# Kernel optimization log

Measured on AMD Instinct MI355X. Metric: run time of the kernel, lower is better.

Reference implementation:

```python
import jax, jax.numpy as jnp
import numpy as np

NUM_EDGE_TYPES = 38
NUM_NODE_TYPES = 4
HIDDEN = 64
HOPS = 4
N_NODES = 100_000
N_EDGES = 1_600_000


def setup_inputs() -> dict:
    key = jax.random.key(0)
    ks = jax.random.split(key, 7)
    in_dim = NUM_EDGE_TYPES + 2 * NUM_NODE_TYPES  # 46
    return {
        "edge_index": jax.random.randint(ks[0], (2, N_EDGES), 0, N_NODES),
        "edge_type": jax.random.randint(ks[1], (N_EDGES,), 0, NUM_EDGE_TYPES),
        "node_type": jax.random.randint(ks[2], (N_NODES,), 0, NUM_NODE_TYPES),
        "W1": jax.random.normal(ks[3], (in_dim, HIDDEN), dtype=jnp.float32) * 0.1,
        "b1": jax.random.normal(ks[4], (HIDDEN,), dtype=jnp.float32) * 0.1,
        "W2": jax.random.normal(ks[5], (HIDDEN, 1), dtype=jnp.float32) * 0.1,
        "b2": jax.random.normal(ks[6], (1,), dtype=jnp.float32) * 0.1,
    }


def reference(edge_index, edge_type, node_type, W1, b1, W2, b2):
    src, dst = edge_index[0], edge_index[1]  # PyG: x_j = x[edge_index[0]], aggregate at edge_index[1]
    head_type = node_type[src]
    tail_type = node_type[dst]
    # Linear over concat of three one-hots == sum of three gathered weight rows + bias.
    h = (W1[edge_type]
         + W1[NUM_EDGE_TYPES + head_type]
         + W1[NUM_EDGE_TYPES + NUM_NODE_TYPES + tail_type]
         + b1)                                   # [E, HIDDEN]
    h = jax.nn.gelu(h)
    edge_emb = jax.nn.sigmoid(h @ W2 + b2)       # [E, 1]

    num_nodes = node_type.shape[0]
    aggr = jnp.zeros((num_nodes, 1), dtype=edge_emb.dtype)
    for _ in range(HOPS):
        msg = aggr[src] + edge_emb               # gather + add, [E, 1]
        aggr = jax.ops.segment_sum(msg, dst, num_segments=num_nodes)  # scatter-add
    return aggr
```

## Files before the change

kernel.cpp:

```cpp
#include <hip/hip_runtime.h>

#define NUM_EDGE_TYPES 38
#define NUM_NODE_TYPES 4
#define HIDDEN 64
#define TABLE_SIZE (NUM_EDGE_TYPES * NUM_NODE_TYPES * NUM_NODE_TYPES)
#define SRC_BITS 17
#define SRC_MASK ((1 << SRC_BITS) - 1)
#define BSHIFT 8
#define BNODES 256
#define MAXB 512
#define CHUNK 4096
#define PB 512
#define HB 1024
#define CAPC 6144

__global__ void partition_kernel(const int* __restrict__ src, const int* __restrict__ dst,
                                 const int* __restrict__ etype, int* __restrict__ cursor,
                                 int* __restrict__ pack, int E, int nbk, int cap) {
    __shared__ int hist[MAXB];
    __shared__ int locCur[MAXB];
    for (int i = threadIdx.x; i < nbk; i += PB) hist[i] = 0;
    __syncthreads();
    int start = blockIdx.x * CHUNK;
    int end = min(start + CHUNK, E);
    if (end - start == CHUNK) {
        int j = start + threadIdx.x;
        int d[8], s[8], et[8], slot[8];
#pragma unroll
        for (int k = 0; k < 8; ++k) d[k] = dst[j + k * PB];
#pragma unroll
        for (int k = 0; k < 8; ++k) atomicAdd(&hist[d[k] >> BSHIFT], 1);
        __syncthreads();
        for (int i = threadIdx.x; i < nbk; i += PB) {
            int h = hist[i];
            locCur[i] = h ? i * cap + atomicAdd(&cursor[i], h) : 0;
        }
        __syncthreads();
#pragma unroll
        for (int k = 0; k < 8; ++k) s[k] = src[j + k * PB];
#pragma unroll
        for (int k = 0; k < 8; ++k) et[k] = etype[j + k * PB];
#pragma unroll
        for (int k = 0; k < 8; ++k) slot[k] = atomicAdd(&locCur[d[k] >> BSHIFT], 1);
#pragma unroll
        for (int k = 0; k < 8; ++k)
            pack[slot[k]] = (et[k] << (SRC_BITS + 8)) | ((d[k] & (BNODES - 1)) << SRC_BITS) | s[k];
    } else {
        for (int j = start + threadIdx.x; j < end; j += PB)
            atomicAdd(&hist[dst[j] >> BSHIFT], 1);
        __syncthreads();
        for (int i = threadIdx.x; i < nbk; i += PB) {
            int h = hist[i];
            locCur[i] = h ? i * cap + atomicAdd(&cursor[i], h) : 0;
        }
        __syncthreads();
        for (int j = start + threadIdx.x; j < end; j += PB) {
            int d = dst[j];
            int slot = atomicAdd(&locCur[d >> BSHIFT], 1);
            pack[slot] = (etype[j] << (SRC_BITS + 8)) | ((d & (BNODES - 1)) << SRC_BITS) | src[j];
        }
    }
}

__global__ void sort_base_kernel(int* __restrict__ pack, const int* __restrict__ cursor,
                                 const int* __restrict__ ntype,
                                 const float* __restrict__ W1, const float* __restrict__ b1,
                                 const float* __restrict__ W2, const float* __restrict__ b2,
                                 float* __restrict__ base, int* __restrict__ nodeOffG,
                                 int N, int cap) {
    __shared__ int sortedL[CAPC];
    __shared__ float tbl[TABLE_SIZE];
    __shared__ int nodeCnt[BNODES];
    __shared__ int nodeOff[BNODES + 1];
    __shared__ unsigned char ntLoc[BNODES];
    int b = blockIdx.x;
    int node0 = b << BSHIFT;
    int tid = threadIdx.x;
    int st = b * cap;
    int c = cursor[b];
    c = min(c, cap);

    if (tid < TABLE_SIZE) {
        int i = tid;
        int et = i >> 4, ht = (i >> 2) & 3, tt = i & 3;
        const float* r0 = W1 + et * HIDDEN;
        const float* r1 = W1 + (NUM_EDGE_TYPES + ht) * HIDDEN;
        const float* r2 = W1 + (NUM_EDGE_TYPES + NUM_NODE_TYPES + tt) * HIDDEN;
        float acc = b2[0];
#pragma unroll 8
        for (int k = 0; k < HIDDEN; ++k) {
            float h = r0[k] + r1[k] + r2[k] + b1[k];
            float u = 0.7978845608028654f * (h + 0.044715f * h * h * h);
            float g = 0.5f * h * (1.0f + tanhf(u));
            acc += g * W2[k];
        }
        tbl[i] = 1.0f / (1.0f + expf(-acc));
    }
    if (tid < BNODES) {
        nodeCnt[tid] = 0;
        int n = node0 + tid;
        ntLoc[tid] = (n < N) ? (unsigned char)ntype[n] : 0;
    }
    __syncthreads();

    for (int j = tid; j < c; j += HB)
        atomicAdd(&nodeCnt[(pack[st + j] >> SRC_BITS) & (BNODES - 1)], 1);
    __syncthreads();

    if (tid < 64) {
        int lane = tid;
        int v0 = nodeCnt[lane * 4], v1 = nodeCnt[lane * 4 + 1];
        int v2 = nodeCnt[lane * 4 + 2], v3 = nodeCnt[lane * 4 + 3];
        int s = v0 + v1 + v2 + v3;
        int inc = s;
        for (int d = 1; d < 64; d <<= 1) {
            int t = __shfl_up(inc, d, 64);
            if (lane >= d) inc += t;
        }
        int excl = inc - s;
        nodeOff[lane * 4]     = excl;
        nodeOff[lane * 4 + 1] = excl + v0;
        nodeOff[lane * 4 + 2] = excl + v0 + v1;
        nodeOff[lane * 4 + 3] = excl + v0 + v1 + v2;
        if (lane == 63) nodeOff[BNODES] = inc;
    }
    __syncthreads();
    if (tid < BNODES) nodeCnt[tid] = 0;
    __syncthreads();

    for (int j = tid; j < c; j += HB) {
        int p = pack[st + j];
        int dl = (p >> SRC_BITS) & (BNODES - 1);
        int r = atomicAdd(&nodeCnt[dl], 1);
        sortedL[nodeOff[dl] + r] = p;
    }
    __syncthreads();

    for (int j = tid; j < c; j += HB) pack[st + j] = sortedL[j];
    if (tid < BNODES) nodeOffG[(b << BSHIFT) + tid] = nodeOff[tid];

    int node = tid >> 2, l = tid & 3;
    int lo = nodeOff[node], hi = nodeOff[node + 1];
    int nt = ntLoc[node];
    float s = 0.0f;
    int j = lo + l;
    for (; j + 4 < hi; j += 8) {
        int p0 = sortedL[j], p1 = sortedL[j + 4];
        int i0 = ((((unsigned)p0) >> (SRC_BITS + 8)) << 4) | (ntype[p0 & SRC_MASK] << 2) | nt;
        int i1 = ((((unsigned)p1) >> (SRC_BITS + 8)) << 4) | (ntype[p1 & SRC_MASK] << 2) | nt;
        s += tbl[i0] + tbl[i1];
    }
    if (j < hi) {
        int p = sortedL[j];
        s += tbl[((((unsigned)p) >> (SRC_BITS + 8)) << 4) | (ntype[p & SRC_MASK] << 2) | nt];
    }
    s += __shfl_xor(s, 1, 64);
    s += __shfl_xor(s, 2, 64);
    int n = node0 + node;
    if (l == 0 && n < N) base[n] = s;
}

__global__ void hop_csr_kernel(const int* __restrict__ pack, const int* __restrict__ nodeOffG,
                               const int* __restrict__ cursor, const float* __restrict__ base,
                               const float* __restrict__ prev, float* __restrict__ out,
                               int N, int cap) {
    __shared__ int off[BNODES + 1];
    int b = blockIdx.x;
    int tid = threadIdx.x;
    int st = b * cap;
    if (tid < BNODES) off[tid] = nodeOffG[(b << BSHIFT) + tid];
    if (tid == 0) off[BNODES] = min(cursor[b], cap);
    __syncthreads();
    int node = tid >> 2, l = tid & 3;
    int lo = off[node], hi = off[node + 1];
    float s = 0.0f;
    int j = st + lo + l;
    int hiG = st + hi;
    for (; j + 4 < hiG; j += 8) {
        int p0 = pack[j], p1 = pack[j + 4];
        s += prev[p0 & SRC_MASK] + prev[p1 & SRC_MASK];
    }
    if (j < hiG) s += prev[pack[j] & SRC_MASK];
    s += __shfl_xor(s, 1, 64);
    s += __shfl_xor(s, 2, 64);
    int n = (b << BSHIFT) + node;
    if (l == 0 && n < N) out[n] = base[n] + s;
}

__global__ void table_kernel(const float* __restrict__ W1, const float* __restrict__ b1,
                             const float* __restrict__ W2, const float* __restrict__ b2,
                             float* __restrict__ table) {
    int i = blockIdx.x * blockDim.x + threadIdx.x;
    if (i >= TABLE_SIZE) return;
    int et = i >> 4, ht = (i >> 2) & 3, tt = i & 3;
    const float* r0 = W1 + et * HIDDEN;
    const float* r1 = W1 + (NUM_EDGE_TYPES + ht) * HIDDEN;
    const float* r2 = W1 + (NUM_EDGE_TYPES + NUM_NODE_TYPES + tt) * HIDDEN;
    float acc = b2[0];
#pragma unroll 8
    for (int k = 0; k < HIDDEN; ++k) {
        float h = r0[k] + r1[k] + r2[k] + b1[k];
        float u = 0.7978845608028654f * (h + 0.044715f * h * h * h);
        float g = 0.5f * h * (1.0f + tanhf(u));
        acc += g * W2[k];
    }
    table[i] = 1.0f / (1.0f + expf(-acc));
}

__global__ void edge_base_kernel(const int* __restrict__ src, const int* __restrict__ dst,
                                 const int* __restrict__ etype, const int* __restrict__ ntype,
                                 const float* __restrict__ table, float* __restrict__ base, int E) {
    __shared__ float tbl[TABLE_SIZE];
    for (int i = threadIdx.x; i < TABLE_SIZE; i += blockDim.x) tbl[i] = table[i];
    __syncthreads();
    int e = blockIdx.x * blockDim.x + threadIdx.x;
    if (e >= E) return;
    int s = src[e];
    int d = dst[e];
    int idx = (etype[e] << 4) | (ntype[s] << 2) | ntype[d];
    atomicAdd(base + d, tbl[idx]);
}

__global__ void copy_kernel(const float* __restrict__ in, float* __restrict__ out, int N) {
    int i = blockIdx.x * blockDim.x + threadIdx.x;
    if (i < N) out[i] = in[i];
}

__global__ void edge_hop_kernel(const int* __restrict__ src, const int* __restrict__ dst,
                                const float* __restrict__ prev, float* __restrict__ next, int E) {
    int e = blockIdx.x * blockDim.x + threadIdx.x;
    if (e >= E) return;
    atomicAdd(next + dst[e], prev[src[e]]);
}

extern "C" void kernel_launch(void* const* d_in, const int* in_sizes, int n_in,
                              void* d_out, int out_size, void* d_ws, size_t ws_size,
                              hipStream_t stream) {
    const int* edge_index = (const int*)d_in[0];
    const int* etype      = (const int*)d_in[1];
    const int* ntype      = (const int*)d_in[2];
    const float* W1       = (const float*)d_in[3];
    const float* b1       = (const float*)d_in[4];
    const float* W2       = (const float*)d_in[5];
    const float* b2       = (const float*)d_in[6];

    const int E = in_sizes[1];
    const int N = in_sizes[2];
    const int* src = edge_index;
    const int* dst = edge_index + E;
    float* out = (float*)d_out;

    const int nbk = (N + BNODES - 1) >> BSHIFT;
    const int nChunks = (E + CHUNK - 1) / CHUNK;

    int cap = ((E / (nbk > 0 ? nbk : 1)) * 3 / 2 + 255) & ~255;
    if (cap < 512) cap = 512;
    size_t packElems = (size_t)nbk * cap;

    size_t need = (packElems + MAXB + (size_t)nbk * BNODES + (size_t)3 * N) * 4 + 256;

    if (ws_size >= need && nbk <= MAXB && cap <= CAPC) {
        int* pack     = (int*)d_ws;
        int* cursor   = pack + packElems;
        int* nodeOffG = cursor + MAXB;
        float* base   = (float*)(nodeOffG + (size_t)nbk * BNODES);
        float* bufA   = base + N;
        float* bufB   = bufA + N;

        hipMemsetAsync(cursor, 0, (size_t)nbk * sizeof(int), stream);

        partition_kernel<<<nChunks, PB, 0, stream>>>(src, dst, etype, cursor, pack, E, nbk, cap);
        sort_base_kernel<<<nbk, HB, 0, stream>>>(pack, cursor, ntype, W1, b1, W2, b2,
                                                 base, nodeOffG, N, cap);
        hop_csr_kernel<<<nbk, HB, 0, stream>>>(pack, nodeOffG, cursor, base, base, bufA, N, cap);
        hop_csr_kernel<<<nbk, HB, 0, stream>>>(pack, nodeOffG, cursor, base, bufA, bufB, N, cap);
        hop_csr_kernel<<<nbk, HB, 0, stream>>>(pack, nodeOffG, cursor, base, bufB, out, N, cap);
    } else {
        float* table = (float*)d_ws;
        float* base  = table + 1024;
        float* bufA  = base + N;
        float* bufB  = bufA + N;
        const int eb = (E + 255) / 256;
        const int nb = (N + 255) / 256;

        hipMemsetAsync(base, 0, (size_t)N * sizeof(float), stream);
        table_kernel<<<(TABLE_SIZE + 255) / 256, 256, 0, stream>>>(W1, b1, W2, b2, table);

        edge_base_kernel<<<eb, 256, 0, stream>>>(src, dst, etype, ntype, table, base, E);
        copy_kernel<<<nb, 256, 0, stream>>>(base, bufA, N);
        edge_hop_kernel<<<eb, 256, 0, stream>>>(src, dst, base, bufA, E);
        copy_kernel<<<nb, 256, 0, stream>>>(base, bufB, N);
        edge_hop_kernel<<<eb, 256, 0, stream>>>(src, dst, bufA, bufB, E);
        copy_kernel<<<nb, 256, 0, stream>>>(base, out, N);
        edge_hop_kernel<<<eb, 256, 0, stream>>>(src, dst, bufB, out, E);
    }
}
```

Before: 155.1 us.

## Fuse sort, base and hop kernels into one cooperative persistent kernel

Replaces the sort_base kernel and three hop_csr launches with a single cooperative kernel that keeps each bucket's sorted edge list in shared memory and separates hops with grid-wide syncs. This removes three kernel launches and the global write and re-read of the sorted pack and node offsets. In exchange it relies on cooperative launch support and all 391 blocks being co-resident (512 threads, about 26KB shared each), and it uses half as many threads per bucket with 2 lanes per node. The table computation is factored into a shared device helper.

New measurement: 326.0 us. +110.2%, slower.

```diff
diff --git a/kernel.cpp b/kernel.cpp
--- a/kernel.cpp
+++ b/kernel.cpp
@@ -1,4 +1,7 @@
 #include <hip/hip_runtime.h>
+#include <hip/hip_cooperative_groups.h>
+
+namespace cg = cooperative_groups;
 
 #define NUM_EDGE_TYPES 38
 #define NUM_NODE_TYPES 4
@@ -12,7 +15,27 @@
 #define CHUNK 4096
 #define PB 512
 #define HB 1024
+#define MB 512
 #define CAPC 6144
+
+__device__ __forceinline__ float table_entry(int i, const float* __restrict__ W1,
+                                             const float* __restrict__ b1,
+                                             const float* __restrict__ W2,
+                                             const float* __restrict__ b2) {
+    int et = i >> 4, ht = (i >> 2) & 3, tt = i & 3;
+    const float* r0 = W1 + et * HIDDEN;
+    const float* r1 = W1 + (NUM_EDGE_TYPES + ht) * HIDDEN;
+    const float* r2 = W1 + (NUM_EDGE_TYPES + NUM_NODE_TYPES + tt) * HIDDEN;
+    float acc = b2[0];
+#pragma unroll 8
+    for (int k = 0; k < HIDDEN; ++k) {
+        float h = r0[k] + r1[k] + r2[k] + b1[k];
+        float u = 0.7978845608028654f * (h + 0.044715f * h * h * h);
+        float g = 0.5f * h * (1.0f + tanhf(u));
+        acc += g * W2[k];
+    }
+    return 1.0f / (1.0f + expf(-acc));
+}
 
 __global__ void partition_kernel(const int* __restrict__ src, const int* __restrict__ dst,
                                  const int* __restrict__ etype, int* __restrict__ cursor,
@@ -59,6 +82,112 @@
             int slot = atomicAdd(&locCur[d >> BSHIFT], 1);
             pack[slot] = (etype[j] << (SRC_BITS + 8)) | ((d & (BNODES - 1)) << SRC_BITS) | src[j];
         }
+    }
+}
+
+__global__ __launch_bounds__(MB, 4)
+void mega_kernel(const int* __restrict__ pack, const int* __restrict__ cursor,
+                 const int* __restrict__ ntype,
+                 const float* __restrict__ W1, const float* __restrict__ b1,
+                 const float* __restrict__ W2, const float* __restrict__ b2,
+                 float* __restrict__ base, float* __restrict__ bufA,
+                 float* __restrict__ bufB, float* __restrict__ out, int N, int cap) {
+    cg::grid_group grid = cg::this_grid();
+    __shared__ int sortedL[CAPC];
+    __shared__ float tbl[TABLE_SIZE];
+    __shared__ int nodeCnt[BNODES];
+    __shared__ int nodeOff[BNODES + 1];
+    __shared__ unsigned char ntLoc[BNODES];
+    __shared__ float baseLoc[BNODES];
+    int b = blockIdx.x;
+    int tid = threadIdx.x;
+    int node0 = b << BSHIFT;
+    int st = b * cap;
+    int c = min(cursor[b], cap);
+
+    for (int i = tid; i < TABLE_SIZE; i += MB) tbl[i] = table_entry(i, W1, b1, W2, b2);
+    if (tid < BNODES) {
+        nodeCnt[tid] = 0;
+        int n = node0 + tid;
+        ntLoc[tid] = (n < N) ? (unsigned char)ntype[n] : 0;
+    }
+    __syncthreads();
+
+    for (int j = tid; j < c; j += MB)
+        atomicAdd(&nodeCnt[(pack[st + j] >> SRC_BITS) & (BNODES - 1)], 1);
+    __syncthreads();
+
+    if (tid < 64) {
+        int lane = tid;
+        int v0 = nodeCnt[lane * 4], v1 = nodeCnt[lane * 4 + 1];
+        int v2 = nodeCnt[lane * 4 + 2], v3 = nodeCnt[lane * 4 + 3];
+        int s = v0 + v1 + v2 + v3;
+        int inc = s;
+        for (int d = 1; d < 64; d <<= 1) {
+            int t = __shfl_up(inc, d, 64);
+            if (lane >= d) inc += t;
+        }
+        int excl = inc - s;
+        nodeOff[lane * 4]     = excl;
+        nodeOff[lane * 4 + 1] = excl + v0;
+        nodeOff[lane * 4 + 2] = excl + v0 + v1;
+        nodeOff[lane * 4 + 3] = excl + v0 + v1 + v2;
+        if (lane == 63) nodeOff[BNODES] = inc;
+    }
+    __syncthreads();
+    if (tid < BNODES) nodeCnt[tid] = 0;
+    __syncthreads();
+
+    for (int j = tid; j < c; j += MB) {
+        int p = pack[st + j];
+        int dl = (p >> SRC_BITS) & (BNODES - 1);
+        int r = atomicAdd(&nodeCnt[dl], 1);
+        sortedL[nodeOff[dl] + r] = p;
+    }
+    __syncthreads();
+
+    int node = tid >> 1, l = tid & 1;
+    int lo = nodeOff[node], hi = nodeOff[node + 1];
+    {
+        int nt = ntLoc[node];
+        float s = 0.0f;
+        int j = lo + l;
+        for (; j + 2 < hi; j += 4) {
+            int p0 = sortedL[j], p1 = sortedL[j + 2];
+            s += tbl[((((unsigned)p0) >> (SRC_BITS + 8)) << 4) | (ntype[p0 & SRC_MASK] << 2) | nt]
+               + tbl[((((unsigned)p1) >> (SRC_BITS + 8)) << 4) | (ntype[p1 & SRC_MASK] << 2) | nt];
+        }
+        if (j < hi) {
+            int p = sortedL[j];
+            s += tbl[((((unsigned)p) >> (SRC_BITS + 8)) << 4) | (ntype[p & SRC_MASK] << 2) | nt];
+        }
+        s += __shfl_xor(s, 1, 64);
+        if (l == 0) {
+            baseLoc[node] = s;
+            int n = node0 + node;
+            if (n < N) base[n] = s;
+        }
+    }
+    grid.sync();
+
+    const float* prevArr[3] = {base, bufA, bufB};
+    float* outArr[3] = {bufA, bufB, out};
+#pragma unroll
+    for (int h = 0; h < 3; ++h) {
+        const float* __restrict__ prev = prevArr[h];
+        float s = 0.0f;
+        int j = lo + l;
+        for (; j + 2 < hi; j += 4) {
+            int p0 = sortedL[j], p1 = sortedL[j + 2];
+            s += prev[p0 & SRC_MASK] + prev[p1 & SRC_MASK];
+        }
+        if (j < hi) s += prev[sortedL[j] & SRC_MASK];
+        s += __shfl_xor(s, 1, 64);
+        if (l == 0) {
+            int n = node0 + node;
+            if (n < N) outArr[h][n] = baseLoc[node] + s;
+        }
+        if (h < 2) grid.sync();
     }
 }
 
@@ -77,36 +206,18 @@
     int node0 = b << BSHIFT;
     int tid = threadIdx.x;
     int st = b * cap;
-    int c = cursor[b];
-    c = min(c, cap);
-
-    if (tid < TABLE_SIZE) {
-        int i = tid;
-        int et = i >> 4, ht = (i >> 2) & 3, tt = i & 3;
-        const float* r0 = W1 + et * HIDDEN;
-        const float* r1 = W1 + (NUM_EDGE_TYPES + ht) * HIDDEN;
-        const float* r2 = W1 + (NUM_EDGE_TYPES + NUM_NODE_TYPES + tt) * HIDDEN;
-        float acc = b2[0];
-#pragma unroll 8
-        for (int k = 0; k < HIDDEN; ++k) {
-            float h = r0[k] + r1[k] + r2[k] + b1[k];
-            float u = 0.7978845608028654f * (h + 0.044715f * h * h * h);
-            float g = 0.5f * h * (1.0f + tanhf(u));
-            acc += g * W2[k];
-        }
-        tbl[i] = 1.0f / (1.0f + expf(-acc));
-    }
+    int c = min(cursor[b], cap);
+
+    if (tid < TABLE_SIZE) tbl[tid] = table_entry(tid, W1, b1, W2, b2);
     if (tid < BNODES) {
         nodeCnt[tid] = 0;
         int n = node0 + tid;
         ntLoc[tid] = (n < N) ? (unsigned char)ntype[n] : 0;
     }
     __syncthreads();
-
     for (int j = tid; j < c; j += HB)
         atomicAdd(&nodeCnt[(pack[st + j] >> SRC_BITS) & (BNODES - 1)], 1);
     __syncthreads();
-
     if (tid < 64) {
         int lane = tid;
         int v0 = nodeCnt[lane * 4], v1 = nodeCnt[lane * 4 + 1];
@@ -127,7 +238,6 @@
     __syncthreads();
     if (tid < BNODES) nodeCnt[tid] = 0;
     __syncthreads();
-
     for (int j = tid; j < c; j += HB) {
         int p = pack[st + j];
         int dl = (p >> SRC_BITS) & (BNODES - 1);
@@ -135,7 +245,6 @@
         sortedL[nodeOff[dl] + r] = p;
     }
     __syncthreads();
-
     for (int j = tid; j < c; j += HB) pack[st + j] = sortedL[j];
     if (tid < BNODES) nodeOffG[(b << BSHIFT) + tid] = nodeOff[tid];
 
@@ -146,9 +255,8 @@
     int j = lo + l;
     for (; j + 4 < hi; j += 8) {
         int p0 = sortedL[j], p1 = sortedL[j + 4];
-        int i0 = ((((unsigned)p0) >> (SRC_BITS + 8)) << 4) | (ntype[p0 & SRC_MASK] << 2) | nt;
-        int i1 = ((((unsigned)p1) >> (SRC_BITS + 8)) << 4) | (ntype[p1 & SRC_MASK] << 2) | nt;
-        s += tbl[i0] + tbl[i1];
+        s += tbl[((((unsigned)p0) >> (SRC_BITS + 8)) << 4) | (ntype[p0 & SRC_MASK] << 2) | nt]
+           + tbl[((((unsigned)p1) >> (SRC_BITS + 8)) << 4) | (ntype[p1 & SRC_MASK] << 2) | nt];
     }
     if (j < hi) {
         int p = sortedL[j];
@@ -191,20 +299,7 @@
                              const float* __restrict__ W2, const float* __restrict__ b2,
                              float* __restrict__ table) {
     int i = blockIdx.x * blockDim.x + threadIdx.x;
-    if (i >= TABLE_SIZE) return;
-    int et = i >> 4, ht = (i >> 2) & 3, tt = i & 3;
-    const float* r0 = W1 + et * HIDDEN;
-    const float* r1 = W1 + (NUM_EDGE_TYPES + ht) * HIDDEN;
-    const float* r2 = W1 + (NUM_EDGE_TYPES + NUM_NODE_TYPES + tt) * HIDDEN;
-    float acc = b2[0];
-#pragma unroll 8
-    for (int k = 0; k < HIDDEN; ++k) {
-        float h = r0[k] + r1[k] + r2[k] + b1[k];
-        float u = 0.7978845608028654f * (h + 0.044715f * h * h * h);
-        float g = 0.5f * h * (1.0f + tanhf(u));
-        acc += g * W2[k];
-    }
-    table[i] = 1.0f / (1.0f + expf(-acc));
+    if (i < TABLE_SIZE) table[i] = table_entry(i, W1, b1, W2, b2);
 }
 
 __global__ void edge_base_kernel(const int* __restrict__ src, const int* __restrict__ dst,
@@ -268,13 +363,27 @@
         float* bufB   = bufA + N;
 
         hipMemsetAsync(cursor, 0, (size_t)nbk * sizeof(int), stream);
-
         partition_kernel<<<nChunks, PB, 0, stream>>>(src, dst, etype, cursor, pack, E, nbk, cap);
-        sort_base_kernel<<<nbk, HB, 0, stream>>>(pack, cursor, ntype, W1, b1, W2, b2,
-                                                 base, nodeOffG, N, cap);
-        hop_csr_kernel<<<nbk, HB, 0, stream>>>(pack, nodeOffG, cursor, base, base, bufA, N, cap);
-        hop_csr_kernel<<<nbk, HB, 0, stream>>>(pack, nodeOffG, cursor, base, bufA, bufB, N, cap);
-        hop_csr_kernel<<<nbk, HB, 0, stream>>>(pack, nodeOffG, cursor, base, bufB, out, N, cap);
+
+        int coop = 0, dev = 0;
+        hipGetDevice(&dev);
+        hipDeviceGetAttribute(&coop, hipDeviceAttributeCooperativeLaunch, dev);
+
+        if (coop && nbk <= 512) {
+            int N_ = N, cap_ = cap;
+            void* args[] = {(void*)&pack, (void*)&cursor, (void*)&ntype,
+                            (void*)&W1, (void*)&b1, (void*)&W2, (void*)&b2,
+                            (void*)&base, (void*)&bufA, (void*)&bufB, (void*)&out,
+                            (void*)&N_, (void*)&cap_};
+            hipLaunchCooperativeKernel((const void*)mega_kernel, dim3(nbk), dim3(MB),
+                                       args, 0, stream);
+        } else {
+            sort_base_kernel<<<nbk, HB, 0, stream>>>(pack, cursor, ntype, W1, b1, W2, b2,
+                                                     base, nodeOffG, N, cap);
+            hop_csr_kernel<<<nbk, HB, 0, stream>>>(pack, nodeOffG, cursor, base, base, bufA, N, cap);
+            hop_csr_kernel<<<nbk, HB, 0, stream>>>(pack, nodeOffG, cursor, base, bufA, bufB, N, cap);
+            hop_csr_kernel<<<nbk, HB, 0, stream>>>(pack, nodeOffG, cursor, base, bufB, out, N, cap);
+        }
     } else {
         float* table = (float*)d_ws;
         float* base  = table + 1024;
```

## Split hop blocks in half, precompute edge table, smaller partition chunks

Applied to the files above, without the earlier changes.

The sigmoid/GELU table is now computed once by a separate kernel instead of redundantly in every sort block, and sort blocks just copy it into shared memory. Hop kernels now launch two 512-thread blocks per 256-node bucket, which gives the scheduler more blocks to spread across CUs. The partition chunk size is halved so more blocks run with fewer edges each. This adds one kernel launch and more global cursor atomics in exchange.

Measured after the change: 157.2 us. No clear change (+1.3%).

```diff
diff --git a/kernel.cpp b/kernel.cpp
--- a/kernel.cpp
+++ b/kernel.cpp
@@ -9,10 +9,36 @@
 #define BSHIFT 8
 #define BNODES 256
 #define MAXB 512
-#define CHUNK 4096
+#define CHUNK 2048
 #define PB 512
 #define HB 1024
 #define CAPC 6144
+
+__device__ __forceinline__ float table_entry(int i, const float* __restrict__ W1,
+                                             const float* __restrict__ b1,
+                                             const float* __restrict__ W2,
+                                             const float* __restrict__ b2) {
+    int et = i >> 4, ht = (i >> 2) & 3, tt = i & 3;
+    const float* r0 = W1 + et * HIDDEN;
+    const float* r1 = W1 + (NUM_EDGE_TYPES + ht) * HIDDEN;
+    const float* r2 = W1 + (NUM_EDGE_TYPES + NUM_NODE_TYPES + tt) * HIDDEN;
+    float acc = b2[0];
+#pragma unroll 8
+    for (int k = 0; k < HIDDEN; ++k) {
+        float h = r0[k] + r1[k] + r2[k] + b1[k];
+        float u = 0.7978845608028654f * (h + 0.044715f * h * h * h);
+        float g = 0.5f * h * (1.0f + tanhf(u));
+        acc += g * W2[k];
+    }
+    return 1.0f / (1.0f + expf(-acc));
+}
+
+__global__ void table_kernel(const float* __restrict__ W1, const float* __restrict__ b1,
+                             const float* __restrict__ W2, const float* __restrict__ b2,
+                             float* __restrict__ table) {
+    int i = blockIdx.x * blockDim.x + threadIdx.x;
+    if (i < TABLE_SIZE) table[i] = table_entry(i, W1, b1, W2, b2);
+}
 
 __global__ void partition_kernel(const int* __restrict__ src, const int* __restrict__ dst,
                                  const int* __restrict__ etype, int* __restrict__ cursor,
@@ -25,11 +51,11 @@
     int end = min(start + CHUNK, E);
     if (end - start == CHUNK) {
         int j = start + threadIdx.x;
-        int d[8], s[8], et[8], slot[8];
-#pragma unroll
-        for (int k = 0; k < 8; ++k) d[k] = dst[j + k * PB];
-#pragma unroll
-        for (int k = 0; k < 8; ++k) atomicAdd(&hist[d[k] >> BSHIFT], 1);
+        int d[4], s[4], et[4], slot[4];
+#pragma unroll
+        for (int k = 0; k < 4; ++k) d[k] = dst[j + k * PB];
+#pragma unroll
+        for (int k = 0; k < 4; ++k) atomicAdd(&hist[d[k] >> BSHIFT], 1);
         __syncthreads();
         for (int i = threadIdx.x; i < nbk; i += PB) {
             int h = hist[i];
@@ -37,13 +63,13 @@
         }
         __syncthreads();
 #pragma unroll
-        for (int k = 0; k < 8; ++k) s[k] = src[j + k * PB];
-#pragma unroll
-        for (int k = 0; k < 8; ++k) et[k] = etype[j + k * PB];
-#pragma unroll
-        for (int k = 0; k < 8; ++k) slot[k] = atomicAdd(&locCur[d[k] >> BSHIFT], 1);
-#pragma unroll
-        for (int k = 0; k < 8; ++k)
+        for (int k = 0; k < 4; ++k) s[k] = src[j + k * PB];
+#pragma unroll
+        for (int k = 0; k < 4; ++k) et[k] = etype[j + k * PB];
+#pragma unroll
+        for (int k = 0; k < 4; ++k) slot[k] = atomicAdd(&locCur[d[k] >> BSHIFT], 1);
+#pragma unroll
+        for (int k = 0; k < 4; ++k)
             pack[slot[k]] = (et[k] << (SRC_BITS + 8)) | ((d[k] & (BNODES - 1)) << SRC_BITS) | s[k];
     } else {
         for (int j = start + threadIdx.x; j < end; j += PB)
@@ -63,9 +89,7 @@
 }
 
 __global__ void sort_base_kernel(int* __restrict__ pack, const int* __restrict__ cursor,
-                                 const int* __restrict__ ntype,
-                                 const float* __restrict__ W1, const float* __restrict__ b1,
-                                 const float* __restrict__ W2, const float* __restrict__ b2,
+                                 const int* __restrict__ ntype, const float* __restrict__ table,
                                  float* __restrict__ base, int* __restrict__ nodeOffG,
                                  int N, int cap) {
     __shared__ int sortedL[CAPC];
@@ -77,25 +101,9 @@
     int node0 = b << BSHIFT;
     int tid = threadIdx.x;
     int st = b * cap;
-    int c = cursor[b];
-    c = min(c, cap);
-
-    if (tid < TABLE_SIZE) {
-        int i = tid;
-        int et = i >> 4, ht = (i >> 2) & 3, tt = i & 3;
-        const float* r0 = W1 + et * HIDDEN;
-        const float* r1 = W1 + (NUM_EDGE_TYPES + ht) * HIDDEN;
-        const float* r2 = W1 + (NUM_EDGE_TYPES + NUM_NODE_TYPES + tt) * HIDDEN;
-        float acc = b2[0];
-#pragma unroll 8
-        for (int k = 0; k < HIDDEN; ++k) {
-            float h = r0[k] + r1[k] + r2[k] + b1[k];
-            float u = 0.7978845608028654f * (h + 0.044715f * h * h * h);
-            float g = 0.5f * h * (1.0f + tanhf(u));
-            acc += g * W2[k];
-        }
-        tbl[i] = 1.0f / (1.0f + expf(-acc));
-    }
+    int c = min(cursor[b], cap);
+
+    if (tid < TABLE_SIZE) tbl[tid] = table[tid];
     if (tid < BNODES) {
         nodeCnt[tid] = 0;
         int n = node0 + tid;
@@ -146,9 +154,8 @@
     int j = lo + l;
     for (; j + 4 < hi; j += 8) {
         int p0 = sortedL[j], p1 = sortedL[j + 4];
-        int i0 = ((((unsigned)p0) >> (SRC_BITS + 8)) << 4) | (ntype[p0 & SRC_MASK] << 2) | nt;
-        int i1 = ((((unsigned)p1) >> (SRC_BITS + 8)) << 4) | (ntype[p1 & SRC_MASK] << 2) | nt;
-        s += tbl[i0] + tbl[i1];
+        s += tbl[((((unsigned)p0) >> (SRC_BITS + 8)) << 4) | (ntype[p0 & SRC_MASK] << 2) | nt]
+           + tbl[((((unsigned)p1) >> (SRC_BITS + 8)) << 4) | (ntype[p1 & SRC_MASK] << 2) | nt];
     }
     if (j < hi) {
         int p = sortedL[j];
@@ -160,16 +167,21 @@
     if (l == 0 && n < N) base[n] = s;
 }
 
-__global__ void hop_csr_kernel(const int* __restrict__ pack, const int* __restrict__ nodeOffG,
-                               const int* __restrict__ cursor, const float* __restrict__ base,
-                               const float* __restrict__ prev, float* __restrict__ out,
-                               int N, int cap) {
-    __shared__ int off[BNODES + 1];
-    int b = blockIdx.x;
+__global__ __launch_bounds__(512)
+void hop_csr_kernel(const int* __restrict__ pack, const int* __restrict__ nodeOffG,
+                    const int* __restrict__ cursor, const float* __restrict__ base,
+                    const float* __restrict__ prev, float* __restrict__ out,
+                    int N, int cap) {
+    __shared__ int off[129];
+    int blk = blockIdx.x;
+    int b = blk >> 1;
+    int half = blk & 1;
     int tid = threadIdx.x;
     int st = b * cap;
-    if (tid < BNODES) off[tid] = nodeOffG[(b << BSHIFT) + tid];
-    if (tid == 0) off[BNODES] = min(cursor[b], cap);
+    int nodeBase = (b << BSHIFT) + half * 128;
+    if (tid < 128) off[tid] = nodeOffG[(b << BSHIFT) + half * 128 + tid];
+    else if (tid == 128)
+        off[128] = half ? min(cursor[b], cap) : nodeOffG[(b << BSHIFT) + 128];
     __syncthreads();
     int node = tid >> 2, l = tid & 3;
     int lo = off[node], hi = off[node + 1];
@@ -183,28 +195,8 @@
     if (j < hiG) s += prev[pack[j] & SRC_MASK];
     s += __shfl_xor(s, 1, 64);
     s += __shfl_xor(s, 2, 64);
-    int n = (b << BSHIFT) + node;
+    int n = nodeBase + node;
     if (l == 0 && n < N) out[n] = base[n] + s;
-}
-
-__global__ void table_kernel(const float* __restrict__ W1, const float* __restrict__ b1,
-                             const float* __restrict__ W2, const float* __restrict__ b2,
-                             float* __restrict__ table) {
-    int i = blockIdx.x * blockDim.x + threadIdx.x;
-    if (i >= TABLE_SIZE) return;
-    int et = i >> 4, ht = (i >> 2) & 3, tt = i & 3;
-    const float* r0 = W1 + et * HIDDEN;
-    const float* r1 = W1 + (NUM_EDGE_TYPES + ht) * HIDDEN;
-    const float* r2 = W1 + (NUM_EDGE_TYPES + NUM_NODE_TYPES + tt) * HIDDEN;
-    float acc = b2[0];
-#pragma unroll 8
-    for (int k = 0; k < HIDDEN; ++k) {
-        float h = r0[k] + r1[k] + r2[k] + b1[k];
-        float u = 0.7978845608028654f * (h + 0.044715f * h * h * h);
-        float g = 0.5f * h * (1.0f + tanhf(u));
-        acc += g * W2[k];
-    }
-    table[i] = 1.0f / (1.0f + expf(-acc));
 }
 
 __global__ void edge_base_kernel(const int* __restrict__ src, const int* __restrict__ dst,
@@ -257,24 +249,24 @@
     if (cap < 512) cap = 512;
     size_t packElems = (size_t)nbk * cap;
 
-    size_t need = (packElems + MAXB + (size_t)nbk * BNODES + (size_t)3 * N) * 4 + 256;
+    size_t need = (packElems + MAXB + (size_t)nbk * BNODES + 1024 + (size_t)3 * N) * 4 + 256;
 
     if (ws_size >= need && nbk <= MAXB && cap <= CAPC) {
         int* pack     = (int*)d_ws;
         int* cursor   = pack + packElems;
         int* nodeOffG = cursor + MAXB;
-        float* base   = (float*)(nodeOffG + (size_t)nbk * BNODES);
+        float* table  = (float*)(nodeOffG + (size_t)nbk * BNODES);
+        float* base   = table + 1024;
         float* bufA   = base + N;
         float* bufB   = bufA + N;
 
         hipMemsetAsync(cursor, 0, (size_t)nbk * sizeof(int), stream);
-
+        table_kernel<<<(TABLE_SIZE + 255) / 256, 256, 0, stream>>>(W1, b1, W2, b2, table);
         partition_kernel<<<nChunks, PB, 0, stream>>>(src, dst, etype, cursor, pack, E, nbk, cap);
-        sort_base_kernel<<<nbk, HB, 0, stream>>>(pack, cursor, ntype, W1, b1, W2, b2,
-                                                 base, nodeOffG, N, cap);
-        hop_csr_kernel<<<nbk, HB, 0, stream>>>(pack, nodeOffG, cursor, base, base, bufA, N, cap);
-        hop_csr_kernel<<<nbk, HB, 0, stream>>>(pack, nodeOffG, cursor, base, bufA, bufB, N, cap);
-        hop_csr_kernel<<<nbk, HB, 0, stream>>>(pack, nodeOffG, cursor, base, bufB, out, N, cap);
+        sort_base_kernel<<<nbk, HB, 0, stream>>>(pack, cursor, ntype, table, base, nodeOffG, N, cap);
+        hop_csr_kernel<<<2 * nbk, 512, 0, stream>>>(pack, nodeOffG, cursor, base, base, bufA, N, cap);
+        hop_csr_kernel<<<2 * nbk, 512, 0, stream>>>(pack, nodeOffG, cursor, base, bufA, bufB, N, cap);
+        hop_csr_kernel<<<2 * nbk, 512, 0, stream>>>(pack, nodeOffG, cursor, base, bufB, out, N, cap);
     } else {
         float* table = (float*)d_ws;
         float* base  = table + 1024;
```
